# Kernel optimization log

Measured on AMD Instinct MI355X. Metric: run time of the kernel, lower is better.

## Reference

```python
import jax, jax.numpy as jnp
import numpy as np

N = 100000
E = 1600000
D = 128


def setup_inputs() -> dict:
    key = jax.random.key(0)
    ks = jax.random.split(key, 6)
    x = jax.random.normal(ks[0], (N, D), dtype=jnp.float32)
    edge_row = jax.random.randint(ks[1], (E,), 0, N)
    edge_col = jax.random.randint(ks[2], (E,), 0, N)
    edge_val = jax.random.uniform(ks[3], (E,), dtype=jnp.float32)
    # Kaiming-ish init for the MLP weights
    W1 = jax.random.normal(ks[4], (D, D), dtype=jnp.float32) * (1.0 / np.sqrt(D))
    W2 = jax.random.normal(ks[5], (D, D), dtype=jnp.float32) * (1.0 / np.sqrt(D))
    b1 = jnp.zeros((D,), dtype=jnp.float32)
    b2 = jnp.zeros((D,), dtype=jnp.float32)
    eps = jnp.zeros((1,), dtype=jnp.float32)  # GIN eps, init 0
    bias = jnp.zeros((D,), dtype=jnp.float32)
    return {"x": x, "edge_row": edge_row, "edge_col": edge_col, "edge_val": edge_val,
            "W1": W1, "b1": b1, "W2": W2, "b2": b2, "eps": eps, "bias": bias}


def reference(x, edge_row, edge_col, edge_val, W1, b1, W2, b2, eps, bias):
    # sparse adj @ x : out[i] = sum_{edges (i,j)} val * x[j]
    agg = jax.ops.segment_sum(edge_val[:, None] * x[edge_col], edge_row, num_segments=N)
    h = (1.0 + eps) * x + agg                     # eps-scaled residual, [N, D]
    h = jax.nn.relu(h @ W1 + b1)                  # MLP layer 1
    h = jax.nn.relu(h @ W2 + b2)                  # MLP layer 2
    out = jax.nn.relu(h + bias)                   # bias + final relu
    return out
```

## Files before the change

kernel.cpp:

```cpp
#include <hip/hip_runtime.h>
#include <stdint.h>


static constexpr int NN = 100000;
static constexpr int NE = 1600000;
static constexpr int NB = 392;
static constexpr int EPB = 4096;
static constexpr int PB = (NE + EPB - 1) / EPB;
static constexpr int BCAP = 8192;
static constexpr int NCVT = (NN * 32) / 1024;
static constexpr int NWB = 16;

typedef float f32x4 __attribute__((ext_vector_type(4)));
typedef short s16x8 __attribute__((ext_vector_type(8)));

__device__ __forceinline__ uint16_t f2bf(float f) {
  uint32_t u = __float_as_uint(f);
  u += 0x7fffu + ((u >> 16) & 1u);
  return (uint16_t)(u >> 16);
}
__device__ __forceinline__ float2 bf2f(uint32_t w) {
  float2 r;
  r.x = __uint_as_float(w << 16);
  r.y = __uint_as_float(w & 0xffff0000u);
  return r;
}

template <int WIDTH>
__device__ __forceinline__ int* scan_inc(int* s0, int* s1, int tid) {
  int* pin = s0;
  int* pout = s1;
  for (int off = 1; off < WIDTH; off <<= 1) {
    if (tid < WIDTH) pout[tid] = pin[tid] + ((tid >= off) ? pin[tid - off] : 0);
    __syncthreads();
    int* tmp = pin; pin = pout; pout = tmp;
  }
  return pin;
}

__global__ __launch_bounds__(1024) void k_prep(const float* __restrict__ x,
                                               uint32_t* __restrict__ xb,
                                               const int* __restrict__ erow,
                                               const int* __restrict__ ecol,
                                               const float* __restrict__ eval,
                                               int2* __restrict__ part,
                                               int* __restrict__ runstart,
                                               const float* __restrict__ W1,
                                               const float* __restrict__ W2,
                                               uint32_t* __restrict__ wbp) {
  __shared__ int hist[NB];
  __shared__ int cur[NB];
  __shared__ int s0[512], s1[512];
  __shared__ int2 stage[EPB];
  int t = threadIdx.x;
  int bid = blockIdx.x;

  if (bid >= PB) {
    int cid = bid - PB;
    if (cid < NCVT) {
      int i = cid * 1024 + t;
      if (i < NN * 32) {
        float4 v = ((const float4*)x)[i];
        uint2 o;
        o.x = (uint32_t)f2bf(v.x) | ((uint32_t)f2bf(v.y) << 16);
        o.y = (uint32_t)f2bf(v.z) | ((uint32_t)f2bf(v.w) << 16);
        ((uint2*)xb)[i] = o;
      }
    } else {
      int flat = (cid - NCVT) * 1024 + t;
      int m = flat >> 13;
      int p = flat & 8191;
      int n = p >> 6;
      int k = (p & 63) * 2;
      const float* Wm = m ? W2 : W1;
      uint32_t lo = f2bf(Wm[k * 128 + n]);
      uint32_t hi = f2bf(Wm[(k + 1) * 128 + n]);
      wbp[(size_t)m * 8192 + n * 64 + (p & 63)] = lo | (hi << 16);
    }
    return;
  }

  int base = bid * EPB;
  int cnt = min(EPB, NE - base);

  if (t < NB) hist[t] = 0;
  __syncthreads();

  int pb[4], pk[4], pv[4];
  #pragma unroll
  for (int j = 0; j < 4; ++j) {
    int i = t + j * 1024;
    pb[j] = -1;
    if (i < cnt) {
      int e = base + i;
      int r = erow[e];
      int b = r >> 8;
      pb[j] = b;
      pk[j] = ecol[e] | ((r & 255) << 17);
      pv[j] = __float_as_int(eval[e]);
      atomicAdd(&hist[b], 1);
    }
  }
  __syncthreads();

  if (t < 512) s0[t] = (t < NB) ? hist[t] : 0;
  __syncthreads();
  int* inc = scan_inc<512>(s0, s1, t);

  if (t < NB) {
    int h = hist[t];
    int st = inc[t] - h;
    cur[t] = st;
    runstart[bid * (NB + 1) + t] = st;
  }
  if (t == 0) runstart[bid * (NB + 1) + NB] = cnt;
  __syncthreads();

  #pragma unroll
  for (int j = 0; j < 4; ++j) {
    if (pb[j] >= 0) {
      int off = atomicAdd(&cur[pb[j]], 1);
      stage[off] = int2{pk[j], pv[j]};
    }
  }
  __syncthreads();

  for (int i = t; i < cnt; i += 1024) part[base + i] = stage[i];
}

__global__ __launch_bounds__(1024) void k_bucket(const int2* __restrict__ part,
                                                 const int* __restrict__ runstart,
                                                 int2* __restrict__ es,
                                                 int* __restrict__ rowptr) {
  __shared__ int cum[PB + 1];
  __shared__ int rbas[PB];
  __shared__ int hist[256];
  __shared__ int rps[256];
  __shared__ int cur[256];
  __shared__ int s0[512], s1[512];
  __shared__ int2 stage[BCAP];
  int b = blockIdx.x, t = threadIdx.x;
  int base_out = b * BCAP;

  int len = 0;
  if (t < PB) {
    int rs = runstart[t * (NB + 1) + b];
    int re = runstart[t * (NB + 1) + b + 1];
    len = re - rs;
    rbas[t] = t * EPB + rs;
  }
  __syncthreads();
  if (t < 512) s0[t] = (t < PB) ? len : 0;
  __syncthreads();
  int* inc1 = scan_inc<512>(s0, s1, t);
  if (t < PB) cum[t] = inc1[t] - len;
  if (t == 0) cum[PB] = inc1[PB - 1];
  if (t < 256) hist[t] = 0;
  __syncthreads();

  int total = cum[PB];

  int pk[8], pv[8];
  #pragma unroll
  for (int j = 0; j < 8; ++j) {
    int s = t + j * 1024;
    pk[j] = -1;
    if (s < total) {
      int lo = 0, hi = PB;
      while (hi - lo > 1) {
        int mid = (lo + hi) >> 1;
        if (cum[mid] <= s) lo = mid; else hi = mid;
      }
      int2 ev = part[rbas[lo] + (s - cum[lo])];
      pk[j] = ev.x; pv[j] = ev.y;
      atomicAdd(&hist[ev.x >> 17], 1);
    }
  }
  __syncthreads();

  if (t < 256) s0[t] = hist[t];
  __syncthreads();
  int* inc2 = scan_inc<256>(s0, s1, t);
  if (t < 256) {
    int ex = inc2[t] - hist[t];
    rps[t] = ex;
    cur[t] = ex;
  }
  __syncthreads();

  if (t < 256) rowptr[b * 257 + t] = base_out + rps[t];
  if (t == 0)  rowptr[b * 257 + 256] = base_out + total;

  #pragma unroll
  for (int j = 0; j < 8; ++j) {
    if (pk[j] >= 0) {
      int rib = pk[j] >> 17;
      int off = atomicAdd(&cur[rib], 1);
      int2 rec = int2{pk[j] & 0x1FFFF, pv[j]};
      if (off < BCAP) stage[off] = rec;
      else es[base_out + off] = rec;
    }
  }
  __syncthreads();

  for (int i = t; i < total; i += 1024) es[base_out + i] = stage[i];
}

__global__ __launch_bounds__(256) void k_agg(const uint32_t* __restrict__ xb,
                                             const int2* __restrict__ es,
                                             const int* __restrict__ rowptr,
                                             const float* __restrict__ eps,
                                             uint32_t* __restrict__ hb) {
  int wid = (blockIdx.x * 256 + threadIdx.x) >> 6;
  int wave = __builtin_amdgcn_readfirstlane(wid);
  int lane = threadIdx.x & 63;
  float e = 1.0f + eps[0];
  float2 h = bf2f(xb[(size_t)wave * 64 + lane]);
  h.x *= e; h.y *= e;
  int rp = (wave >> 8) * 257 + (wave & 255);
  int beg = __builtin_amdgcn_readfirstlane(rowptr[rp]);
  int end = __builtin_amdgcn_readfirstlane(rowptr[rp + 1]);
  for (int k = beg; k < end; k += 16) {
    int scol[16]; float sval[16];
    {
      int2 ev0 = es[k];
      scol[0] = __builtin_amdgcn_readfirstlane(ev0.x);
      sval[0] = __int_as_float(__builtin_amdgcn_readfirstlane(ev0.y));
    }
    #pragma unroll
    for (int j = 1; j < 16; ++j) {
      int2 ev = es[k + j];
      int c = __builtin_amdgcn_readfirstlane(ev.x);
      int vb = __builtin_amdgcn_readfirstlane(ev.y);
      bool live = (k + j < end);
      scol[j] = live ? c : scol[0];
      sval[j] = live ? __int_as_float(vb) : 0.0f;
    }
    uint32_t xw[16];
    #pragma unroll
    for (int j = 0; j < 16; ++j)
      xw[j] = xb[((size_t)scol[j] << 6) + lane];
    #pragma unroll
    for (int j = 0; j < 16; ++j) {
      float2 xv = bf2f(xw[j]);
      h.x = fmaf(sval[j], xv.x, h.x);
      h.y = fmaf(sval[j], xv.y, h.y);
    }
  }
  hb[(size_t)wave * 64 + lane] = (uint32_t)f2bf(h.x) | ((uint32_t)f2bf(h.y) << 16);
}

__global__ __launch_bounds__(256, 3) void k_mlp(const uint16_t* __restrict__ A,
                                                const uint16_t* __restrict__ wb,
                                                const float* __restrict__ b1,
                                                const float* __restrict__ b2,
                                                const float* __restrict__ bias,
                                                float* __restrict__ out, int nrows) {
  __shared__ uint16_t wt[128 * 136];
  __shared__ uint16_t h1[64 * 136];
  int tid = threadIdx.x;

  #pragma unroll
  for (int it = 0; it < 8; ++it) {
    int c = tid + it * 256;
    int r = c >> 4, cc = c & 15;
    *(uint4*)&wt[r * 136 + cc * 8] = *(const uint4*)&wb[r * 128 + cc * 8];
  }
  __syncthreads();

  int wv = tid >> 6, l = tid & 63;
  int m16 = l & 15, qg = l >> 4;
  int r0 = blockIdx.x * 64 + wv * 16;
  int arow = r0 + m16;
  if (arow >= nrows) arow = nrows - 1;

  f32x4 acc[8];
  #pragma unroll
  for (int n0 = 0; n0 < 8; ++n0) acc[n0] = f32x4{0.f, 0.f, 0.f, 0.f};

  #pragma unroll
  for (int k0 = 0; k0 < 128; k0 += 32) {
    s16x8 a = *(const s16x8*)(A + (size_t)arow * 128 + k0 + qg * 8);
    #pragma unroll
    for (int n0 = 0; n0 < 8; ++n0) {
      s16x8 bfr = *(const s16x8*)(&wt[(n0 * 16 + m16) * 136 + k0 + qg * 8]);
      acc[n0] = __builtin_amdgcn_mfma_f32_16x16x32_bf16(a, bfr, acc[n0], 0, 0, 0);
    }
  }

  #pragma unroll
  for (int n0 = 0; n0 < 8; ++n0) {
    int col = n0 * 16 + m16;
    float bb = b1[col];
    #pragma unroll
    for (int j = 0; j < 4; ++j) {
      int lr = wv * 16 + qg * 4 + j;
      h1[lr * 136 + col] = f2bf(fmaxf(acc[n0][j] + bb, 0.0f));
    }
  }
  __syncthreads();

  #pragma unroll
  for (int it = 0; it < 8; ++it) {
    int c = tid + it * 256;
    int r = c >> 4, cc = c & 15;
    *(uint4*)&wt[r * 136 + cc * 8] = *(const uint4*)&wb[16384 + r * 128 + cc * 8];
  }
  #pragma unroll
  for (int n0 = 0; n0 < 8; ++n0) acc[n0] = f32x4{0.f, 0.f, 0.f, 0.f};
  __syncthreads();

  #pragma unroll
  for (int k0 = 0; k0 < 128; k0 += 32) {
    s16x8 a = *(const s16x8*)(&h1[(wv * 16 + m16) * 136 + k0 + qg * 8]);
    #pragma unroll
    for (int n0 = 0; n0 < 8; ++n0) {
      s16x8 bfr = *(const s16x8*)(&wt[(n0 * 16 + m16) * 136 + k0 + qg * 8]);
      acc[n0] = __builtin_amdgcn_mfma_f32_16x16x32_bf16(a, bfr, acc[n0], 0, 0, 0);
    }
  }

  #pragma unroll
  for (int n0 = 0; n0 < 8; ++n0) {
    int col = n0 * 16 + m16;
    float bb = b2[col];
    float b3 = bias[col];
    #pragma unroll
    for (int j = 0; j < 4; ++j) {
      int row = r0 + qg * 4 + j;
      if (row < nrows) {
        float v = fmaxf(fmaxf(acc[n0][j] + bb, 0.0f) + b3, 0.0f);
        out[(size_t)row * 128 + col] = v;
      }
    }
  }
}

extern "C" void kernel_launch(void* const* d_in, const int* in_sizes, int n_in,
                              void* d_out, int out_size, void* d_ws, size_t ws_size,
                              hipStream_t stream) {
  const float* x    = (const float*)d_in[0];
  const int*   erow = (const int*)d_in[1];
  const int*   ecol = (const int*)d_in[2];
  const float* eval = (const float*)d_in[3];
  const float* W1   = (const float*)d_in[4];
  const float* b1   = (const float*)d_in[5];
  const float* W2   = (const float*)d_in[6];
  const float* b2   = (const float*)d_in[7];
  const float* eps  = (const float*)d_in[8];
  const float* bias = (const float*)d_in[9];

  char* w = (char*)d_ws;
  size_t off = 0;
  auto take = [&](size_t bytes) -> void* {
    void* p = w + off;
    off = (off + bytes + 255) & ~(size_t)255;
    return p;
  };
  uint32_t* xb     = (uint32_t*)take((size_t)NN * 64 * 4);
  uint32_t* hb     = (uint32_t*)take((size_t)NN * 64 * 4);
  int2*     part   = (int2*)take((size_t)NE * 8);
  int2*     es     = (int2*)take((size_t)(NB * BCAP + 16) * 8);
  int*      rowptr = (int*)take((size_t)(NB * 257) * 4);
  int*      runst  = (int*)take((size_t)PB * (NB + 1) * 4);
  uint32_t* wb     = (uint32_t*)take((size_t)2 * 8192 * 4);
  (void)ws_size;

  k_prep<<<PB + NCVT + NWB, 1024, 0, stream>>>(x, xb, erow, ecol, eval, part,
                                               runst, W1, W2, wb);
  k_bucket<<<NB, 1024, 0, stream>>>(part, runst, es, rowptr);
  k_agg<<<(NN + 3) / 4, 256, 0, stream>>>(xb, es, rowptr, eps, hb);
  k_mlp<<<(NN + 63) / 64, 256, 0, stream>>>((const uint16_t*)hb,
                                            (const uint16_t*)wb, b1, b2,
                                            bias, (float*)d_out, NN);
}
```

Before: 227.6 us.

## Fuse sparse aggregation and MLP into one kernel via shared-memory tile

```diff
diff --git a/kernel.cpp b/kernel.cpp
--- a/kernel.cpp
+++ b/kernel.cpp
@@ -206,130 +206,130 @@
   for (int i = t; i < total; i += 1024) es[base_out + i] = stage[i];
 }
 
-__global__ __launch_bounds__(256) void k_agg(const uint32_t* __restrict__ xb,
-                                             const int2* __restrict__ es,
-                                             const int* __restrict__ rowptr,
-                                             const float* __restrict__ eps,
-                                             uint32_t* __restrict__ hb) {
-  int wid = (blockIdx.x * 256 + threadIdx.x) >> 6;
-  int wave = __builtin_amdgcn_readfirstlane(wid);
-  int lane = threadIdx.x & 63;
-  float e = 1.0f + eps[0];
-  float2 h = bf2f(xb[(size_t)wave * 64 + lane]);
-  h.x *= e; h.y *= e;
-  int rp = (wave >> 8) * 257 + (wave & 255);
-  int beg = __builtin_amdgcn_readfirstlane(rowptr[rp]);
-  int end = __builtin_amdgcn_readfirstlane(rowptr[rp + 1]);
-  for (int k = beg; k < end; k += 16) {
-    int scol[16]; float sval[16];
-    {
-      int2 ev0 = es[k];
-      scol[0] = __builtin_amdgcn_readfirstlane(ev0.x);
-      sval[0] = __int_as_float(__builtin_amdgcn_readfirstlane(ev0.y));
-    }
-    #pragma unroll
-    for (int j = 1; j < 16; ++j) {
-      int2 ev = es[k + j];
-      int c = __builtin_amdgcn_readfirstlane(ev.x);
-      int vb = __builtin_amdgcn_readfirstlane(ev.y);
-      bool live = (k + j < end);
-      scol[j] = live ? c : scol[0];
-      sval[j] = live ? __int_as_float(vb) : 0.0f;
-    }
-    uint32_t xw[16];
-    #pragma unroll
-    for (int j = 0; j < 16; ++j)
-      xw[j] = xb[((size_t)scol[j] << 6) + lane];
-    #pragma unroll
-    for (int j = 0; j < 16; ++j) {
-      float2 xv = bf2f(xw[j]);
-      h.x = fmaf(sval[j], xv.x, h.x);
-      h.y = fmaf(sval[j], xv.y, h.y);
-    }
-  }
-  hb[(size_t)wave * 64 + lane] = (uint32_t)f2bf(h.x) | ((uint32_t)f2bf(h.y) << 16);
-}
-
-__global__ __launch_bounds__(256, 3) void k_mlp(const uint16_t* __restrict__ A,
-                                                const uint16_t* __restrict__ wb,
-                                                const float* __restrict__ b1,
-                                                const float* __restrict__ b2,
-                                                const float* __restrict__ bias,
-                                                float* __restrict__ out, int nrows) {
+__global__ __launch_bounds__(1024, 8) void k_aggmlp(
+    const uint32_t* __restrict__ xb, const int2* __restrict__ es,
+    const int* __restrict__ rowptr, const float* __restrict__ eps,
+    const uint16_t* __restrict__ wb, const float* __restrict__ b1,
+    const float* __restrict__ b2, const float* __restrict__ bias,
+    float* __restrict__ out, int nrows) {
   __shared__ uint16_t wt[128 * 136];
+  __shared__ uint16_t h0[64 * 136];
   __shared__ uint16_t h1[64 * 136];
   int tid = threadIdx.x;
-
-  #pragma unroll
-  for (int it = 0; it < 8; ++it) {
-    int c = tid + it * 256;
+  int wv = tid >> 6, lane = tid & 63;
+  int r0 = blockIdx.x * 64;
+
+  #pragma unroll
+  for (int it = 0; it < 2; ++it) {
+    int c = tid + it * 1024;
     int r = c >> 4, cc = c & 15;
     *(uint4*)&wt[r * 136 + cc * 8] = *(const uint4*)&wb[r * 128 + cc * 8];
   }
-  __syncthreads();
-
-  int wv = tid >> 6, l = tid & 63;
-  int m16 = l & 15, qg = l >> 4;
-  int r0 = blockIdx.x * 64 + wv * 16;
-  int arow = r0 + m16;
-  if (arow >= nrows) arow = nrows - 1;
-
-  f32x4 acc[8];
-  #pragma unroll
-  for (int n0 = 0; n0 < 8; ++n0) acc[n0] = f32x4{0.f, 0.f, 0.f, 0.f};
-
+
+  float e = 1.0f + eps[0];
+  for (int i = 0; i < 4; ++i) {
+    int lrow = wv * 4 + i;
+    int node = r0 + lrow;
+    uint32_t hw = 0;
+    if (node < nrows) {
+      float2 h = bf2f(xb[(size_t)node * 64 + lane]);
+      h.x *= e; h.y *= e;
+      int rp = (node >> 8) * 257 + (node & 255);
+      int beg = __builtin_amdgcn_readfirstlane(rowptr[rp]);
+      int end = __builtin_amdgcn_readfirstlane(rowptr[rp + 1]);
+      for (int k = beg; k < end; k += 16) {
+        int scol[16]; float sval[16];
+        {
+          int2 ev0 = es[k];
+          scol[0] = __builtin_amdgcn_readfirstlane(ev0.x);
+          sval[0] = __int_as_float(__builtin_amdgcn_readfirstlane(ev0.y));
+        }
+        #pragma unroll
+        for (int j = 1; j < 16; ++j) {
+          int2 ev = es[k + j];
+          int c = __builtin_amdgcn_readfirstlane(ev.x);
+          int vb = __builtin_amdgcn_readfirstlane(ev.y);
+          bool live = (k + j < end);
+          scol[j] = live ? c : scol[0];
+          sval[j] = live ? __int_as_float(vb) : 0.0f;
+        }
+        uint32_t xw[16];
+        #pragma unroll
+        for (int j = 0; j < 16; ++j)
+          xw[j] = xb[((size_t)scol[j] << 6) + lane];
+        #pragma unroll
+        for (int j = 0; j < 16; ++j) {
+          float2 xv = bf2f(xw[j]);
+          h.x = fmaf(sval[j], xv.x, h.x);
+          h.y = fmaf(sval[j], xv.y, h.y);
+        }
+      }
+      hw = (uint32_t)f2bf(h.x) | ((uint32_t)f2bf(h.y) << 16);
+    }
+    ((uint32_t*)h0)[lrow * 68 + lane] = hw;
+  }
+  __syncthreads();
+
+  int rg = wv & 3, cg = wv >> 2;
+  int m16 = lane & 15, qg = lane >> 4;
+
+  f32x4 acc[2];
+  acc[0] = f32x4{0.f, 0.f, 0.f, 0.f};
+  acc[1] = f32x4{0.f, 0.f, 0.f, 0.f};
   #pragma unroll
   for (int k0 = 0; k0 < 128; k0 += 32) {
-    s16x8 a = *(const s16x8*)(A + (size_t)arow * 128 + k0 + qg * 8);
+    s16x8 a = *(const s16x8*)(&h0[(rg * 16 + m16) * 136 + k0 + qg * 8]);
     #pragma unroll
-    for (int n0 = 0; n0 < 8; ++n0) {
+    for (int f = 0; f < 2; ++f) {
+      int n0 = cg * 2 + f;
       s16x8 bfr = *(const s16x8*)(&wt[(n0 * 16 + m16) * 136 + k0 + qg * 8]);
-      acc[n0] = __builtin_amdgcn_mfma_f32_16x16x32_bf16(a, bfr, acc[n0], 0, 0, 0);
-    }
-  }
-
-  #pragma unroll
-  for (int n0 = 0; n0 < 8; ++n0) {
-    int col = n0 * 16 + m16;
+      acc[f] = __builtin_amdgcn_mfma_f32_16x16x32_bf16(a, bfr, acc[f], 0, 0, 0);
+    }
+  }
+
+  #pragma unroll
+  for (int f = 0; f < 2; ++f) {
+    int col = (cg * 2 + f) * 16 + m16;
     float bb = b1[col];
     #pragma unroll
     for (int j = 0; j < 4; ++j) {
-      int lr = wv * 16 + qg * 4 + j;
-      h1[lr * 136 + col] = f2bf(fmaxf(acc[n0][j] + bb, 0.0f));
-    }
-  }
-  __syncthreads();
-
-  #pragma unroll
-  for (int it = 0; it < 8; ++it) {
-    int c = tid + it * 256;
+      int lr = rg * 16 + qg * 4 + j;
+      h1[lr * 136 + col] = f2bf(fmaxf(acc[f][j] + bb, 0.0f));
+    }
+  }
+  __syncthreads();
+
+  #pragma unroll
+  for (int it = 0; it < 2; ++it) {
+    int c = tid + it * 1024;
     int r = c >> 4, cc = c & 15;
     *(uint4*)&wt[r * 136 + cc * 8] = *(const uint4*)&wb[16384 + r * 128 + cc * 8];
   }
-  #pragma unroll
-  for (int n0 = 0; n0 < 8; ++n0) acc[n0] = f32x4{0.f, 0.f, 0.f, 0.f};
+  acc[0] = f32x4{0.f, 0.f, 0.f, 0.f};
+  acc[1] = f32x4{0.f, 0.f, 0.f, 0.f};
   __syncthreads();
 
   #pragma unroll
   for (int k0 = 0; k0 < 128; k0 += 32) {
-    s16x8 a = *(const s16x8*)(&h1[(wv * 16 + m16) * 136 + k0 + qg * 8]);
+    s16x8 a = *(const s16x8*)(&h1[(rg * 16 + m16) * 136 + k0 + qg * 8]);
     #pragma unroll
-    for (int n0 = 0; n0 < 8; ++n0) {
+    for (int f = 0; f < 2; ++f) {
+      int n0 = cg * 2 + f;
       s16x8 bfr = *(const s16x8*)(&wt[(n0 * 16 + m16) * 136 + k0 + qg * 8]);
-      acc[n0] = __builtin_amdgcn_mfma_f32_16x16x32_bf16(a, bfr, acc[n0], 0, 0, 0);
-    }
-  }
-
-  #pragma unroll
-  for (int n0 = 0; n0 < 8; ++n0) {
-    int col = n0 * 16 + m16;
+      acc[f] = __builtin_amdgcn_mfma_f32_16x16x32_bf16(a, bfr, acc[f], 0, 0, 0);
+    }
+  }
+
+  #pragma unroll
+  for (int f = 0; f < 2; ++f) {
+    int col = (cg * 2 + f) * 16 + m16;
     float bb = b2[col];
     float b3 = bias[col];
     #pragma unroll
     for (int j = 0; j < 4; ++j) {
-      int row = r0 + qg * 4 + j;
+      int row = r0 + rg * 16 + qg * 4 + j;
       if (row < nrows) {
-        float v = fmaxf(fmaxf(acc[n0][j] + bb, 0.0f) + b3, 0.0f);
+        float v = fmaxf(fmaxf(acc[f][j] + bb, 0.0f) + b3, 0.0f);
         out[(size_t)row * 128 + col] = v;
       }
     }
@@ -358,7 +358,6 @@
     return p;
   };
   uint32_t* xb     = (uint32_t*)take((size_t)NN * 64 * 4);
-  uint32_t* hb     = (uint32_t*)take((size_t)NN * 64 * 4);
   int2*     part   = (int2*)take((size_t)NE * 8);
   int2*     es     = (int2*)take((size_t)(NB * BCAP + 16) * 8);
   int*      rowptr = (int*)take((size_t)(NB * 257) * 4);
@@ -369,8 +368,7 @@
   k_prep<<<PB + NCVT + NWB, 1024, 0, stream>>>(x, xb, erow, ecol, eval, part,
                                                runst, W1, W2, wb);
   k_bucket<<<NB, 1024, 0, stream>>>(part, runst, es, rowptr);
-  k_agg<<<(NN + 3) / 4, 256, 0, stream>>>(xb, es, rowptr, eps, hb);
-  k_mlp<<<(NN + 63) / 64, 256, 0, stream>>>((const uint16_t*)hb,
-                                            (const uint16_t*)wb, b1, b2,
-                                            bias, (float*)d_out, NN);
-}
+  k_aggmlp<<<(NN + 63) / 64, 1024, 0, stream>>>(xb, es, rowptr, eps,
+                                                (const uint16_t*)wb, b1, b2,
+                                                bias, (float*)d_out, NN);
+}
```

New measurement: 231.5 us. No clear change (+1.7%).

## Fuse edge bucketing and aggregation into one kernel using LDS-staged edges

Applied to the files above, without the earlier changes.

```diff
diff --git a/kernel.cpp b/kernel.cpp
--- a/kernel.cpp
+++ b/kernel.cpp
@@ -128,10 +128,12 @@
   for (int i = t; i < cnt; i += 1024) part[base + i] = stage[i];
 }
 
-__global__ __launch_bounds__(1024) void k_bucket(const int2* __restrict__ part,
-                                                 const int* __restrict__ runstart,
-                                                 int2* __restrict__ es,
-                                                 int* __restrict__ rowptr) {
+__global__ __launch_bounds__(1024) void k_buckagg(const uint32_t* __restrict__ xb,
+                                                  const int2* __restrict__ part,
+                                                  const int* __restrict__ runstart,
+                                                  const float* __restrict__ eps,
+                                                  uint32_t* __restrict__ hb,
+                                                  int nrows) {
   __shared__ int cum[PB + 1];
   __shared__ int rbas[PB];
   __shared__ int hist[256];
@@ -140,7 +142,6 @@
   __shared__ int s0[512], s1[512];
   __shared__ int2 stage[BCAP];
   int b = blockIdx.x, t = threadIdx.x;
-  int base_out = b * BCAP;
 
   int len = 0;
   if (t < PB) {
@@ -188,66 +189,55 @@
   }
   __syncthreads();
 
-  if (t < 256) rowptr[b * 257 + t] = base_out + rps[t];
-  if (t == 0)  rowptr[b * 257 + 256] = base_out + total;
-
   #pragma unroll
   for (int j = 0; j < 8; ++j) {
     if (pk[j] >= 0) {
       int rib = pk[j] >> 17;
       int off = atomicAdd(&cur[rib], 1);
-      int2 rec = int2{pk[j] & 0x1FFFF, pv[j]};
-      if (off < BCAP) stage[off] = rec;
-      else es[base_out + off] = rec;
-    }
-  }
-  __syncthreads();
-
-  for (int i = t; i < total; i += 1024) es[base_out + i] = stage[i];
-}
-
-__global__ __launch_bounds__(256) void k_agg(const uint32_t* __restrict__ xb,
-                                             const int2* __restrict__ es,
-                                             const int* __restrict__ rowptr,
-                                             const float* __restrict__ eps,
-                                             uint32_t* __restrict__ hb) {
-  int wid = (blockIdx.x * 256 + threadIdx.x) >> 6;
-  int wave = __builtin_amdgcn_readfirstlane(wid);
-  int lane = threadIdx.x & 63;
+      if (off < BCAP) stage[off] = int2{pk[j] & 0x1FFFF, pv[j]};
+    }
+  }
+  __syncthreads();
+
+  int wv = t >> 6, lane = t & 63;
   float e = 1.0f + eps[0];
-  float2 h = bf2f(xb[(size_t)wave * 64 + lane]);
-  h.x *= e; h.y *= e;
-  int rp = (wave >> 8) * 257 + (wave & 255);
-  int beg = __builtin_amdgcn_readfirstlane(rowptr[rp]);
-  int end = __builtin_amdgcn_readfirstlane(rowptr[rp + 1]);
-  for (int k = beg; k < end; k += 16) {
-    int scol[16]; float sval[16];
-    {
-      int2 ev0 = es[k];
-      scol[0] = __builtin_amdgcn_readfirstlane(ev0.x);
-      sval[0] = __int_as_float(__builtin_amdgcn_readfirstlane(ev0.y));
-    }
-    #pragma unroll
-    for (int j = 1; j < 16; ++j) {
-      int2 ev = es[k + j];
-      int c = __builtin_amdgcn_readfirstlane(ev.x);
-      int vb = __builtin_amdgcn_readfirstlane(ev.y);
-      bool live = (k + j < end);
-      scol[j] = live ? c : scol[0];
-      sval[j] = live ? __int_as_float(vb) : 0.0f;
-    }
-    uint32_t xw[16];
-    #pragma unroll
-    for (int j = 0; j < 16; ++j)
-      xw[j] = xb[((size_t)scol[j] << 6) + lane];
-    #pragma unroll
-    for (int j = 0; j < 16; ++j) {
-      float2 xv = bf2f(xw[j]);
-      h.x = fmaf(sval[j], xv.x, h.x);
-      h.y = fmaf(sval[j], xv.y, h.y);
-    }
-  }
-  hb[(size_t)wave * 64 + lane] = (uint32_t)f2bf(h.x) | ((uint32_t)f2bf(h.y) << 16);
+  for (int i = 0; i < 16; ++i) {
+    int tr = wv * 16 + i;
+    int node = b * 256 + tr;
+    if (node >= nrows) break;
+    float2 h = bf2f(xb[(size_t)node * 64 + lane]);
+    h.x *= e; h.y *= e;
+    int beg = __builtin_amdgcn_readfirstlane(rps[tr]);
+    int end = __builtin_amdgcn_readfirstlane(cur[tr]);
+    for (int k = beg; k < end; k += 16) {
+      int scol[16]; float sval[16];
+      {
+        int2 ev0 = stage[k];
+        scol[0] = __builtin_amdgcn_readfirstlane(ev0.x);
+        sval[0] = __int_as_float(__builtin_amdgcn_readfirstlane(ev0.y));
+      }
+      #pragma unroll
+      for (int j = 1; j < 16; ++j) {
+        int2 ev = stage[k + j];
+        int c = __builtin_amdgcn_readfirstlane(ev.x);
+        int vb = __builtin_amdgcn_readfirstlane(ev.y);
+        bool live = (k + j < end);
+        scol[j] = live ? c : scol[0];
+        sval[j] = live ? __int_as_float(vb) : 0.0f;
+      }
+      uint32_t xw[16];
+      #pragma unroll
+      for (int j = 0; j < 16; ++j)
+        xw[j] = xb[((size_t)scol[j] << 6) + lane];
+      #pragma unroll
+      for (int j = 0; j < 16; ++j) {
+        float2 xv = bf2f(xw[j]);
+        h.x = fmaf(sval[j], xv.x, h.x);
+        h.y = fmaf(sval[j], xv.y, h.y);
+      }
+    }
+    hb[(size_t)node * 64 + lane] = (uint32_t)f2bf(h.x) | ((uint32_t)f2bf(h.y) << 16);
+  }
 }
 
 __global__ __launch_bounds__(256, 3) void k_mlp(const uint16_t* __restrict__ A,
@@ -360,16 +350,13 @@
   uint32_t* xb     = (uint32_t*)take((size_t)NN * 64 * 4);
   uint32_t* hb     = (uint32_t*)take((size_t)NN * 64 * 4);
   int2*     part   = (int2*)take((size_t)NE * 8);
-  int2*     es     = (int2*)take((size_t)(NB * BCAP + 16) * 8);
-  int*      rowptr = (int*)take((size_t)(NB * 257) * 4);
   int*      runst  = (int*)take((size_t)PB * (NB + 1) * 4);
   uint32_t* wb     = (uint32_t*)take((size_t)2 * 8192 * 4);
   (void)ws_size;
 
   k_prep<<<PB + NCVT + NWB, 1024, 0, stream>>>(x, xb, erow, ecol, eval, part,
                                                runst, W1, W2, wb);
-  k_bucket<<<NB, 1024, 0, stream>>>(part, runst, es, rowptr);
-  k_agg<<<(NN + 3) / 4, 256, 0, stream>>>(xb, es, rowptr, eps, hb);
+  k_buckagg<<<NB, 1024, 0, stream>>>(xb, part, runst, eps, hb, NN);
   k_mlp<<<(NN + 63) / 64, 256, 0, stream>>>((const uint16_t*)hb,
                                             (const uint16_t*)wb, b1, b2,
                                             bias, (float*)d_out, NN);
```

Result: slower. 250.5 us (+10.0%).
